# Kernel tuning notes

Measured on AMD Instinct MI355X. Metric: run time of the kernel, lower is better.

## Reference

```python
import jax, jax.numpy as jnp
import numpy as np

B, CI, CO, H, W, K = 8, 256, 256, 64, 64, 3


def _conv(x, w, b, stride, pad):
    y = jax.lax.conv_general_dilated(x, w, (stride, stride), [(pad, pad), (pad, pad)],
                                     dimension_numbers=('NCHW', 'OIHW', 'NCHW'))
    return y + b[None, :, None, None]


def _bn(x, g, b, eps=1e-5):
    m = jnp.mean(x, axis=(0, 2, 3), keepdims=True)
    v = jnp.var(x, axis=(0, 2, 3), keepdims=True)
    return (x - m) * jax.lax.rsqrt(v + eps) * g[None, :, None, None] + b[None, :, None, None]


def _deform_conv(x, offset, mask, w, b, stride=1, pad=1, k=3):
    # Modulated deformable conv v2 (torchvision deform_conv2d semantics).
    Bn, C, Hh, Ww = x.shape
    Ho = (Hh + 2 * pad - k) // stride + 1
    Wo = (Ww + 2 * pad - k) // stride + 1
    kk = jnp.arange(k * k)
    ky = (kk // k).astype(x.dtype)
    kx = (kk % k).astype(x.dtype)
    base_y = (jnp.arange(Ho) * stride - pad).astype(x.dtype)
    base_x = (jnp.arange(Wo) * stride - pad).astype(x.dtype)
    off = offset.reshape(Bn, k * k, 2, Ho, Wo)  # pairs (dy, dx) per kernel tap
    py = base_y[None, None, :, None] + ky[None, :, None, None] + off[:, :, 0]  # [B,K2,Ho,Wo]
    px = base_x[None, None, None, :] + kx[None, :, None, None] + off[:, :, 1]

    def sample(xb, pyb, pxb):  # xb [C,H,W]; pyb/pxb [K2,Ho,Wo]
        y0 = jnp.floor(pyb)
        x0 = jnp.floor(pxb)
        ly = pyb - y0
        lx = pxb - x0
        y0i = y0.astype(jnp.int32)
        x0i = x0.astype(jnp.int32)
        out = jnp.zeros((C, k * k, Ho, Wo), xb.dtype)
        for dy, dx, wgt in ((0, 0, (1 - ly) * (1 - lx)), (0, 1, (1 - ly) * lx),
                            (1, 0, ly * (1 - lx)), (1, 1, ly * lx)):
            yi = y0i + dy
            xi = x0i + dx
            valid = ((yi >= 0) & (yi < Hh) & (xi >= 0) & (xi < Ww)).astype(xb.dtype)
            yc = jnp.clip(yi, 0, Hh - 1)
            xc = jnp.clip(xi, 0, Ww - 1)
            out = out + xb[:, yc, xc] * (wgt * valid)[None]  # zero padding outside
        return out  # [C,K2,Ho,Wo]

    sampled = jax.vmap(sample)(x, py, px)          # [B,C,K2,Ho,Wo]
    sampled = sampled * mask[:, None]              # modulator mask [B,K2,Ho,Wo]
    wk = w.reshape(w.shape[0], C, k * k)
    return jnp.einsum('bcphw,ocp->bohw', sampled, wk) + b[None, :, None, None]


def setup_inputs() -> dict:
    key = jax.random.key(0)
    ks = jax.random.split(key, 16)
    n = jax.random.normal
    return {
        'x': n(ks[0], (B, CI, H, W), jnp.float32),
        'residual': jnp.zeros((B, CI, H, W), jnp.float32),  # unused (overwritten in forward)
        'w1': n(ks[1], (CO, CI, K, K), jnp.float32) * 0.05,
        'b1': n(ks[2], (CO,), jnp.float32) * 0.01,
        'g1': jnp.ones((CO,), jnp.float32),
        'bt1': jnp.zeros((CO,), jnp.float32),
        'w_off': n(ks[3], (2 * K * K, CO, K, K), jnp.float32) * 0.01,
        'b_off': jnp.zeros((2 * K * K,), jnp.float32),
        'w_mod': n(ks[4], (K * K, CO, K, K), jnp.float32) * 0.01,
        'b_mod': jnp.zeros((K * K,), jnp.float32),
        'w_d': n(ks[5], (CO, CO, K, K), jnp.float32) * 0.05,
        'b_d': jnp.zeros((CO,), jnp.float32),
        'g2': jnp.ones((CO,), jnp.float32),
        'bt2': jnp.zeros((CO,), jnp.float32),
        'w_ds': n(ks[6], (CO, CI, 1, 1), jnp.float32) * 0.05,
        'b_ds': jnp.zeros((CO,), jnp.float32),
        'g3': jnp.ones((CO,), jnp.float32),
        'bt3': jnp.zeros((CO,), jnp.float32),
    }


def reference(x, residual, w1, b1, g1, bt1, w_off, b_off, w_mod, b_mod,
              w_d, b_d, g2, bt2, w_ds, b_ds, g3, bt3):
    # residual arg is overwritten by x in the original forward
    out = jax.nn.relu(_bn(_conv(x, w1, b1, 1, 1), g1, bt1))
    offset = _conv(out, w_off, b_off, 1, 1)
    mask = 2.0 * jax.nn.sigmoid(_conv(out, w_mod, b_mod, 1, 1))
    out = _bn(_deform_conv(out, offset, mask, w_d, b_d, 1, 1, K), g2, bt2)
    res = _bn(_conv(x, w_ds, b_ds, 1, 0), g3, bt3)
    return jax.nn.relu(out + res)
```

## Files before the change

### kernel.cpp

```cpp
#include <hip/hip_runtime.h>
#include <math.h>

typedef __attribute__((ext_vector_type(8))) __bf16 bf16x8;
typedef __attribute__((ext_vector_type(4))) float f32x4;

#define PLANE 4096
#define IMG   1048576

__device__ inline ushort f2bf(float f) {
  uint u = __float_as_uint(f);
  u = (u + 0x7fffu + ((u >> 16) & 1u)) >> 16;
  return (ushort)u;
}

union frag_cv { uint4 u; bf16x8 v; };

__global__ void k_prep(const float* __restrict__ w1, const float* __restrict__ wd,
                       const float* __restrict__ woff, const float* __restrict__ wmod,
                       const float* __restrict__ wds,
                       ushort* __restrict__ wb1, ushort* __restrict__ wbd,
                       ushort* __restrict__ wbom, ushort* __restrict__ wbds) {
  int stride = gridDim.x * blockDim.x;
  int t0 = blockIdx.x * blockDim.x + threadIdx.x;
  for (int s = t0; s < 9 * 8 * 256 * 32; s += stride) {
    int kk = s & 31, co = (s >> 5) & 255, cic = (s >> 13) & 7, p = s >> 16;
    int ci = cic * 32 + kk;
    wb1[s] = f2bf(w1[(co * 256 + ci) * 9 + p]);
    wbd[s] = f2bf(wd[(co * 256 + ci) * 9 + p]);
  }
  for (int s = t0; s < 9 * 8 * 32 * 32; s += stride) {
    int kk = s & 31, co = (s >> 5) & 31, cic = (s >> 10) & 7, p = s >> 13;
    int ci = cic * 32 + kk;
    float v = 0.f;
    if (co < 18) v = woff[(co * 256 + ci) * 9 + p];
    else if (co < 27) v = wmod[((co - 18) * 256 + ci) * 9 + p];
    wbom[s] = f2bf(v);
  }
  for (int s = t0; s < 8 * 256 * 32; s += stride) {
    int kk = s & 31, co = (s >> 5) & 255, cic = s >> 13;
    wbds[s] = f2bf(wds[co * 256 + cic * 32 + kk]);
  }
}

__global__ __launch_bounds__(256) void k_x2nhwc(const float* __restrict__ x,
                                                ushort* __restrict__ xn) {
  __shared__ __align__(16) float sT[64 * 68];
  const int h = blockIdx.x, b = blockIdx.y, t = threadIdx.x;
  for (int chunk = 0; chunk < 4; ++chunk) {
    const int c0 = chunk * 64;
    {
      int w4 = (t & 15) * 4, cl = t >> 4;
      #pragma unroll
      for (int i = 0; i < 4; ++i) {
        int c = cl * 4 + i;
        float4 v = *(const float4*)&x[((b * 256 + c0 + c) * 64 + h) * 64 + w4];
        *(float4*)&sT[c * 68 + w4] = v;
      }
    }
    __syncthreads();
    {
      int w = t & 63, cg = t >> 6;
      #pragma unroll
      for (int i = 0; i < 2; ++i) {
        int cg2 = cg * 2 + i;
        uint ou[4];
        #pragma unroll
        for (int k2 = 0; k2 < 4; ++k2) {
          float lo = sT[(cg2 * 8 + k2 * 2) * 68 + w];
          float hi = sT[(cg2 * 8 + k2 * 2 + 1) * 68 + w];
          ou[k2] = (uint)f2bf(lo) | ((uint)f2bf(hi) << 16);
        }
        *(uint4*)&xn[(((b * 64 + h) * 64 + w) * 256) + c0 + cg2 * 8] = *(uint4*)ou;
      }
    }
    __syncthreads();
  }
}

template<int NCO, int NTAP, int MODE>
__global__ __launch_bounds__(256) void k_conv(const ushort* __restrict__ an,
                                              const ushort* __restrict__ wB,
                                              const float* __restrict__ boff,
                                              const float* __restrict__ bmod,
                                              float* __restrict__ out) {
  __shared__ __align__(16) ushort sA[64 * 264];
  __shared__ __align__(16) ushort sB[NCO * 40];
  const int h = blockIdx.x, b = blockIdx.y, t = threadIdx.x;
  const int lane = t & 63, wv = t >> 6;
  constexpr int MF = (NCO == 256) ? 4 : 1;
  constexpr int NF = (NCO == 256) ? 4 : 2;
  const int co_w = (NCO == 256) ? wv * 64 : 0;
  const int m0 = (NCO == 256) ? 0 : wv;
  f32x4 acc[MF][NF];
  #pragma unroll
  for (int m = 0; m < MF; ++m)
    #pragma unroll
    for (int n = 0; n < NF; ++n) acc[m][n] = (f32x4){0.f, 0.f, 0.f, 0.f};

  const int spx = t & 63, seg = t >> 6;
  for (int p = 0; p < NTAP; ++p) {
    {
      int ky = (NTAP == 9) ? p / 3 : 1, kx = (NTAP == 9) ? p % 3 : 1;
      int y = h + ky - 1;
      int sx = spx + kx - 1;
      bool ok = ((unsigned)y < 64u) && ((unsigned)sx < 64u);
      const ushort* src = an + (((b * 64 + y) * 64 + sx) * 256) + seg * 64;
      uint4 z = {0u, 0u, 0u, 0u};
      #pragma unroll
      for (int j = 0; j < 8; ++j) {
        uint4 v = z;
        if (ok) v = *(const uint4*)(src + j * 8);
        *(uint4*)&sA[spx * 264 + seg * 64 + j * 8] = v;
      }
    }
    for (int cic = 0; cic < 8; ++cic) {
      if (t < NCO) {
        const ushort* srcB = wB + ((p * 8 + cic) * NCO + t) * 32;
        #pragma unroll
        for (int j = 0; j < 4; ++j)
          *(uint4*)&sB[t * 40 + j * 8] = *(const uint4*)(srcB + j * 8);
      }
      __syncthreads();
      const int krow = lane >> 4;
      bf16x8 af[MF], bfr[NF];
      #pragma unroll
      for (int m = 0; m < MF; ++m) {
        frag_cv cv;
        cv.u = *(const uint4*)&sA[((m0 + m) * 16 + (lane & 15)) * 264 + cic * 32 + krow * 8];
        af[m] = cv.v;
      }
      #pragma unroll
      for (int n = 0; n < NF; ++n) {
        frag_cv cv;
        cv.u = *(const uint4*)&sB[(co_w + n * 16 + (lane & 15)) * 40 + krow * 8];
        bfr[n] = cv.v;
      }
      #pragma unroll
      for (int m = 0; m < MF; ++m)
        #pragma unroll
        for (int n = 0; n < NF; ++n)
          acc[m][n] = __builtin_amdgcn_mfma_f32_16x16x32_bf16(af[m], bfr[n], acc[m][n], 0, 0, 0);
      __syncthreads();
    }
  }
  const int row0 = (b * 64 + h) * 64;
  if (MODE == 0) {
    #pragma unroll
    for (int m = 0; m < MF; ++m) {
      int pxo = (m0 + m) * 16 + (lane >> 4) * 4;
      #pragma unroll
      for (int n = 0; n < NF; ++n) {
        int co = co_w + n * 16 + (lane & 15);
        #pragma unroll
        for (int r = 0; r < 4; ++r)
          out[(row0 + pxo + r) * 256 + co] = acc[m][n][r];
      }
    }
  } else {
    int pxo = m0 * 16 + (lane >> 4) * 4;
    #pragma unroll
    for (int n = 0; n < NF; ++n) {
      int co = n * 16 + (lane & 15);
      #pragma unroll
      for (int r = 0; r < 4; ++r) {
        float v = acc[0][n][r];
        float o;
        if (co < 18) o = v + boff[co];
        else if (co < 27) { float mm = v + bmod[co - 18]; o = 2.f / (1.f + __expf(-mm)); }
        else o = 0.f;
        out[(row0 + pxo + r) * 32 + co] = o;
      }
    }
  }
}

__global__ __launch_bounds__(256) void k_deform(const ushort* __restrict__ an,
                                                const float* __restrict__ om,
                                                const ushort* __restrict__ wB,
                                                float* __restrict__ out) {
  __shared__ __align__(16) ushort sA[64 * 264];
  __shared__ __align__(16) ushort sB[256 * 40];
  __shared__ __align__(16) float4 sW4[9 * 64];
  __shared__ uchar2 sYX[9 * 64];
  const int h = blockIdx.x, b = blockIdx.y, t = threadIdx.x;
  const int lane = t & 63, wv = t >> 6;
  for (int s = t; s < 576; s += 256) {
    int px = s & 63, p = s >> 6;
    int row = (b * 64 + h) * 64 + px;
    float dy = om[row * 32 + 2 * p];
    float dx = om[row * 32 + 2 * p + 1];
    float mk = om[row * 32 + 18 + p];
    float py = (float)(h + p / 3 - 1) + dy;
    float pxx = (float)(px + p % 3 - 1) + dx;
    float fy = floorf(py), fx = floorf(pxx);
    float ly = py - fy, lx = pxx - fx;
    int y0 = (int)fy, x0 = (int)fx;
    bool vy0 = ((unsigned)y0 < 64u), vy1 = ((unsigned)(y0 + 1) < 64u);
    bool vx0 = ((unsigned)x0 < 64u), vx1 = ((unsigned)(x0 + 1) < 64u);
    float4 wvv;
    wvv.x = (1.f - ly) * (1.f - lx) * mk * ((vy0 && vx0) ? 1.f : 0.f);
    wvv.y = (1.f - ly) * lx * mk * ((vy0 && vx1) ? 1.f : 0.f);
    wvv.z = ly * (1.f - lx) * mk * ((vy1 && vx0) ? 1.f : 0.f);
    wvv.w = ly * lx * mk * ((vy1 && vx1) ? 1.f : 0.f);
    sW4[p * 64 + px] = wvv;
    int yc = min(max(y0, -4), 250), xc = min(max(x0, -4), 250);
    sYX[p * 64 + px] = make_uchar2((unsigned char)(yc + 4), (unsigned char)(xc + 4));
  }
  __syncthreads();
  f32x4 acc[4][4];
  #pragma unroll
  for (int m = 0; m < 4; ++m)
    #pragma unroll
    for (int n = 0; n < 4; ++n) acc[m][n] = (f32x4){0.f, 0.f, 0.f, 0.f};

  const int spx = t & 63, seg = t >> 6;
  const ushort* base = an + (b * PLANE) * 256;
  for (int p = 0; p < 9; ++p) {
    {
      float4 wvv = sW4[p * 64 + spx];
      uchar2 yx = sYX[p * 64 + spx];
      int y0 = (int)yx.x - 4, x0 = (int)yx.y - 4;
      int y0c = min(max(y0, 0), 63), y1c = min(max(y0 + 1, 0), 63);
      int x0c = min(max(x0, 0), 63), x1c = min(max(x0 + 1, 0), 63);
      const ushort* r00 = base + (y0c * 64 + x0c) * 256 + seg * 64;
      const ushort* r01 = base + (y0c * 64 + x1c) * 256 + seg * 64;
      const ushort* r10 = base + (y1c * 64 + x0c) * 256 + seg * 64;
      const ushort* r11 = base + (y1c * 64 + x1c) * 256 + seg * 64;
      #pragma unroll
      for (int j = 0; j < 8; ++j) {
        uint4 c00 = *(const uint4*)(r00 + j * 8);
        uint4 c01 = *(const uint4*)(r01 + j * 8);
        uint4 c10 = *(const uint4*)(r10 + j * 8);
        uint4 c11 = *(const uint4*)(r11 + j * 8);
        uint ou[4];
        #pragma unroll
        for (int q = 0; q < 4; ++q) {
          uint a0 = ((const uint*)&c00)[q], a1 = ((const uint*)&c01)[q];
          uint a2 = ((const uint*)&c10)[q], a3 = ((const uint*)&c11)[q];
          float lo = wvv.x * __uint_as_float(a0 << 16) + wvv.y * __uint_as_float(a1 << 16)
                   + wvv.z * __uint_as_float(a2 << 16) + wvv.w * __uint_as_float(a3 << 16);
          float hi = wvv.x * __uint_as_float(a0 & 0xffff0000u) + wvv.y * __uint_as_float(a1 & 0xffff0000u)
                   + wvv.z * __uint_as_float(a2 & 0xffff0000u) + wvv.w * __uint_as_float(a3 & 0xffff0000u);
          ou[q] = (uint)f2bf(lo) | ((uint)f2bf(hi) << 16);
        }
        *(uint4*)&sA[spx * 264 + seg * 64 + j * 8] = *(uint4*)ou;
      }
    }
    for (int cic = 0; cic < 8; ++cic) {
      {
        const ushort* srcB = wB + ((p * 8 + cic) * 256 + t) * 32;
        #pragma unroll
        for (int j = 0; j < 4; ++j)
          *(uint4*)&sB[t * 40 + j * 8] = *(const uint4*)(srcB + j * 8);
      }
      __syncthreads();
      const int krow = lane >> 4;
      bf16x8 af[4], bfr[4];
      #pragma unroll
      for (int m = 0; m < 4; ++m) {
        frag_cv cv;
        cv.u = *(const uint4*)&sA[(m * 16 + (lane & 15)) * 264 + cic * 32 + krow * 8];
        af[m] = cv.v;
      }
      #pragma unroll
      for (int n = 0; n < 4; ++n) {
        frag_cv cv;
        cv.u = *(const uint4*)&sB[(wv * 64 + n * 16 + (lane & 15)) * 40 + krow * 8];
        bfr[n] = cv.v;
      }
      #pragma unroll
      for (int m = 0; m < 4; ++m)
        #pragma unroll
        for (int n = 0; n < 4; ++n)
          acc[m][n] = __builtin_amdgcn_mfma_f32_16x16x32_bf16(af[m], bfr[n], acc[m][n], 0, 0, 0);
      __syncthreads();
    }
  }
  const int row0 = (b * 64 + h) * 64;
  #pragma unroll
  for (int m = 0; m < 4; ++m) {
    int pxo = m * 16 + (lane >> 4) * 4;
    #pragma unroll
    for (int n = 0; n < 4; ++n) {
      int co = wv * 64 + n * 16 + (lane & 15);
      #pragma unroll
      for (int r = 0; r < 4; ++r)
        out[(row0 + pxo + r) * 256 + co] = acc[m][n][r];
    }
  }
}

__global__ __launch_bounds__(256) void k_statA(const float* __restrict__ t, float* __restrict__ part) {
  const int c = threadIdx.x;
  const int base = blockIdx.x * 128;
  float s1 = 0.f, s2 = 0.f;
  for (int r = 0; r < 128; ++r) {
    float v = t[(base + r) * 256 + c];
    s1 += v; s2 += v * v;
  }
  part[blockIdx.x * 512 + c] = s1;
  part[blockIdx.x * 512 + 256 + c] = s2;
}
__global__ void k_statB(const float* __restrict__ part, const float* __restrict__ g,
                        const float* __restrict__ bt, float* __restrict__ scale,
                        float* __restrict__ shift) {
  const int c = threadIdx.x;
  float s1 = 0.f, s2 = 0.f;
  for (int r = 0; r < 256; ++r) { s1 += part[r * 512 + c]; s2 += part[r * 512 + 256 + c]; }
  const float inv = 1.f / 32768.f;
  float m = s1 * inv;
  float var = s2 * inv - m * m;
  float a = g[c] * rsqrtf(var + 1e-5f);
  scale[c] = a;
  shift[c] = bt[c] - m * a;
}

__global__ void k_bnrelu(const float* __restrict__ t, const float* __restrict__ scale,
                         const float* __restrict__ shift, ushort* __restrict__ o) {
  int stride = gridDim.x * blockDim.x;
  for (int i = blockIdx.x * blockDim.x + threadIdx.x; i < 8388608 / 4; i += stride) {
    float4 v = ((const float4*)t)[i];
    int c0 = (i & 63) * 4;
    float4 s = *(const float4*)&scale[c0];
    float4 sh = *(const float4*)&shift[c0];
    float q0 = fmaxf(v.x * s.x + sh.x, 0.f);
    float q1 = fmaxf(v.y * s.y + sh.y, 0.f);
    float q2 = fmaxf(v.z * s.z + sh.z, 0.f);
    float q3 = fmaxf(v.w * s.w + sh.w, 0.f);
    uint lo = (uint)f2bf(q0) | ((uint)f2bf(q1) << 16);
    uint hi = (uint)f2bf(q2) | ((uint)f2bf(q3) << 16);
    ((uint2*)o)[i] = make_uint2(lo, hi);
  }
}

__global__ __launch_bounds__(256) void k_final(const float* __restrict__ t2, const float* __restrict__ res,
                                               const float* __restrict__ s2p, const float* __restrict__ sh2p,
                                               const float* __restrict__ s3p, const float* __restrict__ sh3p,
                                               float* __restrict__ o) {
  __shared__ __align__(16) float sT[64 * 68];
  const int h = blockIdx.x, b = blockIdx.y, t = threadIdx.x;
  const int row0 = (b * 64 + h) * 64;
  for (int chunk = 0; chunk < 4; ++chunk) {
    const int c0 = chunk * 64;
    {
      int px = t >> 2, s4 = t & 3;
      int rbase = (row0 + px) * 256 + c0 + s4 * 16;
      #pragma unroll
      for (int j = 0; j < 4; ++j) {
        int cl = s4 * 16 + j * 4;
        float4 a = *(const float4*)&t2[rbase + j * 4];
        float4 r = *(const float4*)&res[rbase + j * 4];
        float4 sa = *(const float4*)&s2p[c0 + cl];
        float4 sha = *(const float4*)&sh2p[c0 + cl];
        float4 sb = *(const float4*)&s3p[c0 + cl];
        float4 shb = *(const float4*)&sh3p[c0 + cl];
        sT[(cl + 0) * 68 + px] = fmaxf(a.x * sa.x + sha.x + r.x * sb.x + shb.x, 0.f);
        sT[(cl + 1) * 68 + px] = fmaxf(a.y * sa.y + sha.y + r.y * sb.y + shb.y, 0.f);
        sT[(cl + 2) * 68 + px] = fmaxf(a.z * sa.z + sha.z + r.z * sb.z + shb.z, 0.f);
        sT[(cl + 3) * 68 + px] = fmaxf(a.w * sa.w + sha.w + r.w * sb.w + shb.w, 0.f);
      }
    }
    __syncthreads();
    {
      int cl = t & 63, wseg = t >> 6;
      int obase = ((b * 256 + c0 + cl) * 64 + h) * 64 + wseg * 16;
      #pragma unroll
      for (int j = 0; j < 4; ++j) {
        float4 q;
        q.x = sT[cl * 68 + wseg * 16 + j * 4 + 0];
        q.y = sT[cl * 68 + wseg * 16 + j * 4 + 1];
        q.z = sT[cl * 68 + wseg * 16 + j * 4 + 2];
        q.w = sT[cl * 68 + wseg * 16 + j * 4 + 3];
        *(float4*)&o[obase + j * 4] = q;
      }
    }
    __syncthreads();
  }
}

extern "C" void kernel_launch(void* const* d_in, const int* in_sizes, int n_in,
                              void* d_out, int out_size, void* d_ws, size_t ws_size,
                              hipStream_t stream) {
  const float* x    = (const float*)d_in[0];
  const float* w1   = (const float*)d_in[2];
  const float* g1   = (const float*)d_in[4];
  const float* bt1  = (const float*)d_in[5];
  const float* woff = (const float*)d_in[6];
  const float* boff = (const float*)d_in[7];
  const float* wmod = (const float*)d_in[8];
  const float* bmod = (const float*)d_in[9];
  const float* wd   = (const float*)d_in[10];
  const float* g2   = (const float*)d_in[12];
  const float* bt2  = (const float*)d_in[13];
  const float* wds  = (const float*)d_in[14];
  const float* g3   = (const float*)d_in[16];
  const float* bt3  = (const float*)d_in[17];

  float* ws = (float*)d_ws;
  ushort* wb1  = (ushort*)ws;
  ushort* wbd  = (ushort*)(ws + 294912);
  ushort* wbom = (ushort*)(ws + 589824);
  ushort* wbds = (ushort*)(ws + 626688);
  float*  SC   = ws + 659456;
  float*  part = ws + 661504;
  ushort* xn   = (ushort*)(ws + 792576);
  ushort* out1 = (ushort*)(ws + 4986880);
  float*  t1   = ws + 9181184;
  float*  t2   = ws + 17569792;
  float*  om   = ws + 25958400;
  float*  res  = t1;

  dim3 ghb(64, 8);
  k_prep<<<512, 256, 0, stream>>>(w1, wd, woff, wmod, wds, wb1, wbd, wbom, wbds);
  k_x2nhwc<<<ghb, 256, 0, stream>>>(x, xn);
  k_conv<256, 9, 0><<<ghb, 256, 0, stream>>>(xn, wb1, nullptr, nullptr, t1);
  k_statA<<<256, 256, 0, stream>>>(t1, part);
  k_statB<<<1, 256, 0, stream>>>(part, g1, bt1, SC, SC + 256);
  k_bnrelu<<<2048, 256, 0, stream>>>(t1, SC, SC + 256, out1);
  k_conv<32, 9, 1><<<ghb, 256, 0, stream>>>(out1, wbom, boff, bmod, om);
  k_deform<<<ghb, 256, 0, stream>>>(out1, om, wbd, t2);
  k_statA<<<256, 256, 0, stream>>>(t2, part);
  k_statB<<<1, 256, 0, stream>>>(part, g2, bt2, SC + 512, SC + 768);
  k_conv<256, 1, 0><<<ghb, 256, 0, stream>>>(xn, wbds, nullptr, nullptr, res);
  k_statA<<<256, 256, 0, stream>>>(res, part);
  k_statB<<<1, 256, 0, stream>>>(part, g3, bt3, SC + 1024, SC + 1280);
  k_final<<<ghb, 256, 0, stream>>>(t2, res, SC + 512, SC + 768, SC + 1024, SC + 1280, (float*)d_out);
}
```

Before: 525.6 us.

## Fuse BN stats into conv epilogues, store bf16 intermediates, double-buffer weight tiles

The conv and deform kernels now compute per-block channel sums and sums of squares in their epilogues, which removes the separate k_statA passes. Intermediate activations (t1, t2, res) are stored as bf16 instead of fp32, halving their memory traffic. Weight tiles are double-buffered in shared memory with register prefetch, which cuts one barrier per K-step. The offset/mask conv now processes two rows per block. The risks are extra bf16 rounding of pre-BN values and higher shared memory and register use, which may lower occupancy.

```diff
diff --git a/kernel.cpp b/kernel.cpp
--- a/kernel.cpp
+++ b/kernel.cpp
@@ -77,98 +77,211 @@
   }
 }
 
-template<int NCO, int NTAP, int MODE>
-__global__ __launch_bounds__(256) void k_conv(const ushort* __restrict__ an,
-                                              const ushort* __restrict__ wB,
-                                              const float* __restrict__ boff,
-                                              const float* __restrict__ bmod,
-                                              float* __restrict__ out) {
+template<int NTAP>
+__global__ __launch_bounds__(256) void k_convbig(const ushort* __restrict__ an,
+                                                 const ushort* __restrict__ wB,
+                                                 ushort* __restrict__ ob,
+                                                 float* __restrict__ part) {
   __shared__ __align__(16) ushort sA[64 * 264];
-  __shared__ __align__(16) ushort sB[NCO * 40];
+  __shared__ __align__(16) ushort sB[2][256 * 40];
   const int h = blockIdx.x, b = blockIdx.y, t = threadIdx.x;
   const int lane = t & 63, wv = t >> 6;
-  constexpr int MF = (NCO == 256) ? 4 : 1;
-  constexpr int NF = (NCO == 256) ? 4 : 2;
-  const int co_w = (NCO == 256) ? wv * 64 : 0;
-  const int m0 = (NCO == 256) ? 0 : wv;
-  f32x4 acc[MF][NF];
-  #pragma unroll
-  for (int m = 0; m < MF; ++m)
-    #pragma unroll
-    for (int n = 0; n < NF; ++n) acc[m][n] = (f32x4){0.f, 0.f, 0.f, 0.f};
-
   const int spx = t & 63, seg = t >> 6;
+  f32x4 acc[4][4];
+  #pragma unroll
+  for (int m = 0; m < 4; ++m)
+    #pragma unroll
+    for (int n = 0; n < 4; ++n) acc[m][n] = (f32x4){0.f, 0.f, 0.f, 0.f};
+
+  uint4 aR[8], bR[4];
+  auto loadA = [&](int p) {
+    int ky = (NTAP == 9) ? p / 3 : 1, kx = (NTAP == 9) ? p % 3 : 1;
+    int y = h + ky - 1, sx = spx + kx - 1;
+    bool ok = ((unsigned)y < 64u) && ((unsigned)sx < 64u);
+    const ushort* src = an + (((b * 64 + y) * 64 + sx) * 256) + seg * 64;
+    #pragma unroll
+    for (int j = 0; j < 8; ++j) {
+      uint4 v = {0u, 0u, 0u, 0u};
+      if (ok) v = *(const uint4*)(src + j * 8);
+      aR[j] = v;
+    }
+  };
+  auto writeA = [&]() {
+    #pragma unroll
+    for (int j = 0; j < 8; ++j)
+      *(uint4*)&sA[spx * 264 + seg * 64 + j * 8] = aR[j];
+  };
+  auto loadB = [&](int s) {
+    const ushort* srcB = wB + (s * 256 + t) * 32;
+    #pragma unroll
+    for (int j = 0; j < 4; ++j) bR[j] = *(const uint4*)(srcB + j * 8);
+  };
+  auto writeB = [&](int buf) {
+    #pragma unroll
+    for (int j = 0; j < 4; ++j)
+      *(uint4*)&sB[buf][t * 40 + j * 8] = bR[j];
+  };
+
+  loadA(0); writeA();
+  loadB(0); writeB(0);
+  __syncthreads();
+  int buf = 0;
   for (int p = 0; p < NTAP; ++p) {
-    {
-      int ky = (NTAP == 9) ? p / 3 : 1, kx = (NTAP == 9) ? p % 3 : 1;
-      int y = h + ky - 1;
-      int sx = spx + kx - 1;
+    #pragma unroll
+    for (int cic = 0; cic < 8; ++cic) {
+      const int s = p * 8 + cic;
+      const bool last = (s == NTAP * 8 - 1);
+      const bool tapEnd = (cic == 7) && (p + 1 < NTAP);
+      if (!last) loadB(s + 1);
+      if (tapEnd) loadA(p + 1);
+      const int krow = lane >> 4;
+      bf16x8 af[4], bfr[4];
+      #pragma unroll
+      for (int m = 0; m < 4; ++m) {
+        frag_cv cv;
+        cv.u = *(const uint4*)&sA[(m * 16 + (lane & 15)) * 264 + cic * 32 + krow * 8];
+        af[m] = cv.v;
+      }
+      #pragma unroll
+      for (int n = 0; n < 4; ++n) {
+        frag_cv cv;
+        cv.u = *(const uint4*)&sB[buf][(wv * 64 + n * 16 + (lane & 15)) * 40 + krow * 8];
+        bfr[n] = cv.v;
+      }
+      #pragma unroll
+      for (int m = 0; m < 4; ++m)
+        #pragma unroll
+        for (int n = 0; n < 4; ++n)
+          acc[m][n] = __builtin_amdgcn_mfma_f32_16x16x32_bf16(af[m], bfr[n], acc[m][n], 0, 0, 0);
+      if (!last) writeB(buf ^ 1);
+      __syncthreads();
+      buf ^= 1;
+      if (tapEnd) { writeA(); __syncthreads(); }
+    }
+  }
+  const int row0 = (b * 64 + h) * 64;
+  #pragma unroll
+  for (int m = 0; m < 4; ++m) {
+    int pxo = m * 16 + (lane >> 4) * 4;
+    #pragma unroll
+    for (int n = 0; n < 4; ++n) {
+      int co = wv * 64 + n * 16 + (lane & 15);
+      #pragma unroll
+      for (int r = 0; r < 4; ++r)
+        ob[(row0 + pxo + r) * 256 + co] = f2bf(acc[m][n][r]);
+    }
+  }
+  const int blk = b * 64 + h;
+  #pragma unroll
+  for (int n = 0; n < 4; ++n) {
+    float s1 = 0.f, s2 = 0.f;
+    #pragma unroll
+    for (int m = 0; m < 4; ++m)
+      #pragma unroll
+      for (int r = 0; r < 4; ++r) {
+        float v = acc[m][n][r];
+        s1 += v; s2 += v * v;
+      }
+    s1 += __shfl_xor(s1, 16); s1 += __shfl_xor(s1, 32);
+    s2 += __shfl_xor(s2, 16); s2 += __shfl_xor(s2, 32);
+    if (lane < 16) {
+      int co = wv * 64 + n * 16 + lane;
+      part[blk * 512 + co] = s1;
+      part[blk * 512 + 256 + co] = s2;
+    }
+  }
+}
+
+__global__ __launch_bounds__(256) void k_convom(const ushort* __restrict__ an,
+                                                const ushort* __restrict__ wB,
+                                                const float* __restrict__ boff,
+                                                const float* __restrict__ bmod,
+                                                float* __restrict__ om) {
+  __shared__ __align__(16) ushort sA[128 * 264];
+  __shared__ __align__(16) ushort sB[2][32 * 40];
+  const int h0 = blockIdx.x * 2, b = blockIdx.y, t = threadIdx.x;
+  const int lane = t & 63, wv = t >> 6;
+  const int spx = t & 63, seg = t >> 6;
+  f32x4 acc[2][2];
+  #pragma unroll
+  for (int m = 0; m < 2; ++m)
+    #pragma unroll
+    for (int n = 0; n < 2; ++n) acc[m][n] = (f32x4){0.f, 0.f, 0.f, 0.f};
+
+  uint2 bR;
+  auto stageA = [&](int p) {
+    int ky = p / 3, kx = p % 3;
+    #pragma unroll
+    for (int rr = 0; rr < 2; ++rr) {
+      int y = h0 + rr + ky - 1, sx = spx + kx - 1;
       bool ok = ((unsigned)y < 64u) && ((unsigned)sx < 64u);
       const ushort* src = an + (((b * 64 + y) * 64 + sx) * 256) + seg * 64;
-      uint4 z = {0u, 0u, 0u, 0u};
       #pragma unroll
       for (int j = 0; j < 8; ++j) {
-        uint4 v = z;
+        uint4 v = {0u, 0u, 0u, 0u};
         if (ok) v = *(const uint4*)(src + j * 8);
-        *(uint4*)&sA[spx * 264 + seg * 64 + j * 8] = v;
-      }
-    }
+        *(uint4*)&sA[(rr * 64 + spx) * 264 + seg * 64 + j * 8] = v;
+      }
+    }
+  };
+  auto loadB = [&](int s) { bR = *(const uint2*)(wB + s * 1024 + t * 4); };
+  auto writeB = [&](int buf) {
+    int co = t >> 3, c4 = (t & 7) * 4;
+    *(uint2*)&sB[buf][co * 40 + c4] = bR;
+  };
+
+  stageA(0);
+  loadB(0); writeB(0);
+  __syncthreads();
+  int buf = 0;
+  for (int p = 0; p < 9; ++p) {
+    #pragma unroll
     for (int cic = 0; cic < 8; ++cic) {
-      if (t < NCO) {
-        const ushort* srcB = wB + ((p * 8 + cic) * NCO + t) * 32;
+      const int s = p * 8 + cic;
+      const bool last = (s == 71);
+      const bool tapEnd = (cic == 7) && (p < 8);
+      if (!last) loadB(s + 1);
+      const int krow = lane >> 4;
+      bf16x8 af[2], bfr[2];
+      #pragma unroll
+      for (int m = 0; m < 2; ++m) {
+        frag_cv cv;
+        cv.u = *(const uint4*)&sA[((wv * 2 + m) * 16 + (lane & 15)) * 264 + cic * 32 + krow * 8];
+        af[m] = cv.v;
+      }
+      #pragma unroll
+      for (int n = 0; n < 2; ++n) {
+        frag_cv cv;
+        cv.u = *(const uint4*)&sB[buf][(n * 16 + (lane & 15)) * 40 + krow * 8];
+        bfr[n] = cv.v;
+      }
+      #pragma unroll
+      for (int m = 0; m < 2; ++m)
         #pragma unroll
-        for (int j = 0; j < 4; ++j)
-          *(uint4*)&sB[t * 40 + j * 8] = *(const uint4*)(srcB + j * 8);
-      }
+        for (int n = 0; n < 2; ++n)
+          acc[m][n] = __builtin_amdgcn_mfma_f32_16x16x32_bf16(af[m], bfr[n], acc[m][n], 0, 0, 0);
+      if (!last) writeB(buf ^ 1);
       __syncthreads();
-      const int krow = lane >> 4;
-      bf16x8 af[MF], bfr[NF];
-      #pragma unroll
-      for (int m = 0; m < MF; ++m) {
-        frag_cv cv;
-        cv.u = *(const uint4*)&sA[((m0 + m) * 16 + (lane & 15)) * 264 + cic * 32 + krow * 8];
-        af[m] = cv.v;
-      }
-      #pragma unroll
-      for (int n = 0; n < NF; ++n) {
-        frag_cv cv;
-        cv.u = *(const uint4*)&sB[(co_w + n * 16 + (lane & 15)) * 40 + krow * 8];
-        bfr[n] = cv.v;
-      }
-      #pragma unroll
-      for (int m = 0; m < MF; ++m)
-        #pragma unroll
-        for (int n = 0; n < NF; ++n)
-          acc[m][n] = __builtin_amdgcn_mfma_f32_16x16x32_bf16(af[m], bfr[n], acc[m][n], 0, 0, 0);
-      __syncthreads();
-    }
-  }
-  const int row0 = (b * 64 + h) * 64;
-  if (MODE == 0) {
-    #pragma unroll
-    for (int m = 0; m < MF; ++m) {
-      int pxo = (m0 + m) * 16 + (lane >> 4) * 4;
-      #pragma unroll
-      for (int n = 0; n < NF; ++n) {
-        int co = co_w + n * 16 + (lane & 15);
-        #pragma unroll
-        for (int r = 0; r < 4; ++r)
-          out[(row0 + pxo + r) * 256 + co] = acc[m][n][r];
-      }
-    }
-  } else {
-    int pxo = m0 * 16 + (lane >> 4) * 4;
-    #pragma unroll
-    for (int n = 0; n < NF; ++n) {
+      buf ^= 1;
+      if (tapEnd) { stageA(p + 1); __syncthreads(); }
+    }
+  }
+  #pragma unroll
+  for (int m = 0; m < 2; ++m) {
+    int pxf = (wv * 2 + m) * 16 + (lane >> 4) * 4;
+    #pragma unroll
+    for (int n = 0; n < 2; ++n) {
       int co = n * 16 + (lane & 15);
       #pragma unroll
       for (int r = 0; r < 4; ++r) {
-        float v = acc[0][n][r];
+        float v = acc[m][n][r];
+        int px = pxf + r;
+        int row = (b * 64 + h0 + (px >> 6)) * 64 + (px & 63);
         float o;
         if (co < 18) o = v + boff[co];
         else if (co < 27) { float mm = v + bmod[co - 18]; o = 2.f / (1.f + __expf(-mm)); }
         else o = 0.f;
-        out[(row0 + pxo + r) * 32 + co] = o;
+        om[row * 32 + co] = o;
       }
     }
   }
@@ -177,83 +290,86 @@
 __global__ __launch_bounds__(256) void k_deform(const ushort* __restrict__ an,
                                                 const float* __restrict__ om,
                                                 const ushort* __restrict__ wB,
-                                                float* __restrict__ out) {
+                                                ushort* __restrict__ ob,
+                                                float* __restrict__ part) {
   __shared__ __align__(16) ushort sA[64 * 264];
-  __shared__ __align__(16) ushort sB[256 * 40];
-  __shared__ __align__(16) float4 sW4[9 * 64];
-  __shared__ uchar2 sYX[9 * 64];
+  __shared__ __align__(16) ushort sB[2][256 * 40];
   const int h = blockIdx.x, b = blockIdx.y, t = threadIdx.x;
   const int lane = t & 63, wv = t >> 6;
-  for (int s = t; s < 576; s += 256) {
-    int px = s & 63, p = s >> 6;
-    int row = (b * 64 + h) * 64 + px;
+  const int spx = t & 63, seg = t >> 6;
+  f32x4 acc[4][4];
+  #pragma unroll
+  for (int m = 0; m < 4; ++m)
+    #pragma unroll
+    for (int n = 0; n < 4; ++n) acc[m][n] = (f32x4){0.f, 0.f, 0.f, 0.f};
+
+  const ushort* base = an + (size_t)b * PLANE * 256;
+  const int row = (b * 64 + h) * 64 + spx;
+  uint4 bR[4];
+
+  auto gatherA = [&](int p) {
     float dy = om[row * 32 + 2 * p];
     float dx = om[row * 32 + 2 * p + 1];
     float mk = om[row * 32 + 18 + p];
     float py = (float)(h + p / 3 - 1) + dy;
-    float pxx = (float)(px + p % 3 - 1) + dx;
+    float pxx = (float)(spx + p % 3 - 1) + dx;
     float fy = floorf(py), fx = floorf(pxx);
     float ly = py - fy, lx = pxx - fx;
     int y0 = (int)fy, x0 = (int)fx;
     bool vy0 = ((unsigned)y0 < 64u), vy1 = ((unsigned)(y0 + 1) < 64u);
     bool vx0 = ((unsigned)x0 < 64u), vx1 = ((unsigned)(x0 + 1) < 64u);
-    float4 wvv;
-    wvv.x = (1.f - ly) * (1.f - lx) * mk * ((vy0 && vx0) ? 1.f : 0.f);
-    wvv.y = (1.f - ly) * lx * mk * ((vy0 && vx1) ? 1.f : 0.f);
-    wvv.z = ly * (1.f - lx) * mk * ((vy1 && vx0) ? 1.f : 0.f);
-    wvv.w = ly * lx * mk * ((vy1 && vx1) ? 1.f : 0.f);
-    sW4[p * 64 + px] = wvv;
-    int yc = min(max(y0, -4), 250), xc = min(max(x0, -4), 250);
-    sYX[p * 64 + px] = make_uchar2((unsigned char)(yc + 4), (unsigned char)(xc + 4));
-  }
+    float w00 = (1.f - ly) * (1.f - lx) * mk * ((vy0 && vx0) ? 1.f : 0.f);
+    float w01 = (1.f - ly) * lx * mk * ((vy0 && vx1) ? 1.f : 0.f);
+    float w10 = ly * (1.f - lx) * mk * ((vy1 && vx0) ? 1.f : 0.f);
+    float w11 = ly * lx * mk * ((vy1 && vx1) ? 1.f : 0.f);
+    int y0c = min(max(y0, 0), 63), y1c = min(max(y0 + 1, 0), 63);
+    int x0c = min(max(x0, 0), 63), x1c = min(max(x0 + 1, 0), 63);
+    const ushort* r00 = base + (y0c * 64 + x0c) * 256 + seg * 64;
+    const ushort* r01 = base + (y0c * 64 + x1c) * 256 + seg * 64;
+    const ushort* r10 = base + (y1c * 64 + x0c) * 256 + seg * 64;
+    const ushort* r11 = base + (y1c * 64 + x1c) * 256 + seg * 64;
+    #pragma unroll
+    for (int j = 0; j < 8; ++j) {
+      uint4 c00 = *(const uint4*)(r00 + j * 8);
+      uint4 c01 = *(const uint4*)(r01 + j * 8);
+      uint4 c10 = *(const uint4*)(r10 + j * 8);
+      uint4 c11 = *(const uint4*)(r11 + j * 8);
+      uint ou[4];
+      #pragma unroll
+      for (int q = 0; q < 4; ++q) {
+        uint a0 = ((const uint*)&c00)[q], a1 = ((const uint*)&c01)[q];
+        uint a2 = ((const uint*)&c10)[q], a3 = ((const uint*)&c11)[q];
+        float lo = w00 * __uint_as_float(a0 << 16) + w01 * __uint_as_float(a1 << 16)
+                 + w10 * __uint_as_float(a2 << 16) + w11 * __uint_as_float(a3 << 16);
+        float hi = w00 * __uint_as_float(a0 & 0xffff0000u) + w01 * __uint_as_float(a1 & 0xffff0000u)
+                 + w10 * __uint_as_float(a2 & 0xffff0000u) + w11 * __uint_as_float(a3 & 0xffff0000u);
+        ou[q] = (uint)f2bf(lo) | ((uint)f2bf(hi) << 16);
+      }
+      *(uint4*)&sA[spx * 264 + seg * 64 + j * 8] = *(uint4*)ou;
+    }
+  };
+  auto loadB = [&](int s) {
+    const ushort* srcB = wB + (s * 256 + t) * 32;
+    #pragma unroll
+    for (int j = 0; j < 4; ++j) bR[j] = *(const uint4*)(srcB + j * 8);
+  };
+  auto writeB = [&](int buf) {
+    #pragma unroll
+    for (int j = 0; j < 4; ++j)
+      *(uint4*)&sB[buf][t * 40 + j * 8] = bR[j];
+  };
+
+  gatherA(0);
+  loadB(0); writeB(0);
   __syncthreads();
-  f32x4 acc[4][4];
-  #pragma unroll
-  for (int m = 0; m < 4; ++m)
-    #pragma unroll
-    for (int n = 0; n < 4; ++n) acc[m][n] = (f32x4){0.f, 0.f, 0.f, 0.f};
-
-  const int spx = t & 63, seg = t >> 6;
-  const ushort* base = an + (b * PLANE) * 256;
+  int buf = 0;
   for (int p = 0; p < 9; ++p) {
-    {
-      float4 wvv = sW4[p * 64 + spx];
-      uchar2 yx = sYX[p * 64 + spx];
-      int y0 = (int)yx.x - 4, x0 = (int)yx.y - 4;
-      int y0c = min(max(y0, 0), 63), y1c = min(max(y0 + 1, 0), 63);
-      int x0c = min(max(x0, 0), 63), x1c = min(max(x0 + 1, 0), 63);
-      const ushort* r00 = base + (y0c * 64 + x0c) * 256 + seg * 64;
-      const ushort* r01 = base + (y0c * 64 + x1c) * 256 + seg * 64;
-      const ushort* r10 = base + (y1c * 64 + x0c) * 256 + seg * 64;
-      const ushort* r11 = base + (y1c * 64 + x1c) * 256 + seg * 64;
-      #pragma unroll
-      for (int j = 0; j < 8; ++j) {
-        uint4 c00 = *(const uint4*)(r00 + j * 8);
-        uint4 c01 = *(const uint4*)(r01 + j * 8);
-        uint4 c10 = *(const uint4*)(r10 + j * 8);
-        uint4 c11 = *(const uint4*)(r11 + j * 8);
-        uint ou[4];
-        #pragma unroll
-        for (int q = 0; q < 4; ++q) {
-          uint a0 = ((const uint*)&c00)[q], a1 = ((const uint*)&c01)[q];
-          uint a2 = ((const uint*)&c10)[q], a3 = ((const uint*)&c11)[q];
-          float lo = wvv.x * __uint_as_float(a0 << 16) + wvv.y * __uint_as_float(a1 << 16)
-                   + wvv.z * __uint_as_float(a2 << 16) + wvv.w * __uint_as_float(a3 << 16);
-          float hi = wvv.x * __uint_as_float(a0 & 0xffff0000u) + wvv.y * __uint_as_float(a1 & 0xffff0000u)
-                   + wvv.z * __uint_as_float(a2 & 0xffff0000u) + wvv.w * __uint_as_float(a3 & 0xffff0000u);
-          ou[q] = (uint)f2bf(lo) | ((uint)f2bf(hi) << 16);
-        }
-        *(uint4*)&sA[spx * 264 + seg * 64 + j * 8] = *(uint4*)ou;
-      }
-    }
+    #pragma unroll
     for (int cic = 0; cic < 8; ++cic) {
-      {
-        const ushort* srcB = wB + ((p * 8 + cic) * 256 + t) * 32;
-        #pragma unroll
-        for (int j = 0; j < 4; ++j)
-          *(uint4*)&sB[t * 40 + j * 8] = *(const uint4*)(srcB + j * 8);
-      }
-      __syncthreads();
+      const int s = p * 8 + cic;
+      const bool last = (s == 71);
+      const bool tapEnd = (cic == 7) && (p < 8);
+      if (!last) loadB(s + 1);
       const int krow = lane >> 4;
       bf16x8 af[4], bfr[4];
       #pragma unroll
@@ -265,7 +381,7 @@
       #pragma unroll
       for (int n = 0; n < 4; ++n) {
         frag_cv cv;
-        cv.u = *(const uint4*)&sB[(wv * 64 + n * 16 + (lane & 15)) * 40 + krow * 8];
+        cv.u = *(const uint4*)&sB[buf][(wv * 64 + n * 16 + (lane & 15)) * 40 + krow * 8];
         bfr[n] = cv.v;
       }
       #pragma unroll
@@ -273,7 +389,10 @@
         #pragma unroll
         for (int n = 0; n < 4; ++n)
           acc[m][n] = __builtin_amdgcn_mfma_f32_16x16x32_bf16(af[m], bfr[n], acc[m][n], 0, 0, 0);
+      if (!last) writeB(buf ^ 1);
       __syncthreads();
+      buf ^= 1;
+      if (tapEnd) { gatherA(p + 1); __syncthreads(); }
     }
   }
   const int row0 = (b * 64 + h) * 64;
@@ -285,28 +404,37 @@
       int co = wv * 64 + n * 16 + (lane & 15);
       #pragma unroll
       for (int r = 0; r < 4; ++r)
-        out[(row0 + pxo + r) * 256 + co] = acc[m][n][r];
-    }
-  }
-}
-
-__global__ __launch_bounds__(256) void k_statA(const float* __restrict__ t, float* __restrict__ part) {
-  const int c = threadIdx.x;
-  const int base = blockIdx.x * 128;
-  float s1 = 0.f, s2 = 0.f;
-  for (int r = 0; r < 128; ++r) {
-    float v = t[(base + r) * 256 + c];
-    s1 += v; s2 += v * v;
-  }
-  part[blockIdx.x * 512 + c] = s1;
-  part[blockIdx.x * 512 + 256 + c] = s2;
-}
+        ob[(row0 + pxo + r) * 256 + co] = f2bf(acc[m][n][r]);
+    }
+  }
+  const int blk = b * 64 + h;
+  #pragma unroll
+  for (int n = 0; n < 4; ++n) {
+    float s1 = 0.f, s2 = 0.f;
+    #pragma unroll
+    for (int m = 0; m < 4; ++m)
+      #pragma unroll
+      for (int r = 0; r < 4; ++r) {
+        float v = acc[m][n][r];
+        s1 += v; s2 += v * v;
+      }
+    s1 += __shfl_xor(s1, 16); s1 += __shfl_xor(s1, 32);
+    s2 += __shfl_xor(s2, 16); s2 += __shfl_xor(s2, 32);
+    if (lane < 16) {
+      int co = wv * 64 + n * 16 + lane;
+      part[blk * 512 + co] = s1;
+      part[blk * 512 + 256 + co] = s2;
+    }
+  }
+}
+
+template<int R>
 __global__ void k_statB(const float* __restrict__ part, const float* __restrict__ g,
                         const float* __restrict__ bt, float* __restrict__ scale,
                         float* __restrict__ shift) {
   const int c = threadIdx.x;
   float s1 = 0.f, s2 = 0.f;
-  for (int r = 0; r < 256; ++r) { s1 += part[r * 512 + c]; s2 += part[r * 512 + 256 + c]; }
+  for (int r = 0; r < R; ++r) { s1 += part[r * 512 + c]; s2 += part[r * 512 + 256 + c]; }
   const float inv = 1.f / 32768.f;
   float m = s1 * inv;
   float var = s2 * inv - m * m;
@@ -315,25 +443,34 @@
   shift[c] = bt[c] - m * a;
 }
 
-__global__ void k_bnrelu(const float* __restrict__ t, const float* __restrict__ scale,
+__global__ void k_bnrelu(const ushort* __restrict__ t, const float* __restrict__ scale,
                          const float* __restrict__ shift, ushort* __restrict__ o) {
   int stride = gridDim.x * blockDim.x;
-  for (int i = blockIdx.x * blockDim.x + threadIdx.x; i < 8388608 / 4; i += stride) {
-    float4 v = ((const float4*)t)[i];
-    int c0 = (i & 63) * 4;
-    float4 s = *(const float4*)&scale[c0];
-    float4 sh = *(const float4*)&shift[c0];
-    float q0 = fmaxf(v.x * s.x + sh.x, 0.f);
-    float q1 = fmaxf(v.y * s.y + sh.y, 0.f);
-    float q2 = fmaxf(v.z * s.z + sh.z, 0.f);
-    float q3 = fmaxf(v.w * s.w + sh.w, 0.f);
-    uint lo = (uint)f2bf(q0) | ((uint)f2bf(q1) << 16);
-    uint hi = (uint)f2bf(q2) | ((uint)f2bf(q3) << 16);
-    ((uint2*)o)[i] = make_uint2(lo, hi);
-  }
-}
-
-__global__ __launch_bounds__(256) void k_final(const float* __restrict__ t2, const float* __restrict__ res,
+  for (int i = blockIdx.x * blockDim.x + threadIdx.x; i < 8388608 / 8; i += stride) {
+    uint4 v = ((const uint4*)t)[i];
+    int c0 = (i & 31) * 8;
+    float4 sa = *(const float4*)&scale[c0];
+    float4 sb = *(const float4*)&scale[c0 + 4];
+    float4 ha = *(const float4*)&shift[c0];
+    float4 hb = *(const float4*)&shift[c0 + 4];
+    float e0 = __uint_as_float(v.x << 16), e1 = __uint_as_float(v.x & 0xffff0000u);
+    float e2 = __uint_as_float(v.y << 16), e3 = __uint_as_float(v.y & 0xffff0000u);
+    float e4 = __uint_as_float(v.z << 16), e5 = __uint_as_float(v.z & 0xffff0000u);
+    float e6 = __uint_as_float(v.w << 16), e7 = __uint_as_float(v.w & 0xffff0000u);
+    float q0 = fmaxf(e0 * sa.x + ha.x, 0.f), q1 = fmaxf(e1 * sa.y + ha.y, 0.f);
+    float q2 = fmaxf(e2 * sa.z + ha.z, 0.f), q3 = fmaxf(e3 * sa.w + ha.w, 0.f);
+    float q4 = fmaxf(e4 * sb.x + hb.x, 0.f), q5 = fmaxf(e5 * sb.y + hb.y, 0.f);
+    float q6 = fmaxf(e6 * sb.z + hb.z, 0.f), q7 = fmaxf(e7 * sb.w + hb.w, 0.f);
+    uint4 ou;
+    ou.x = (uint)f2bf(q0) | ((uint)f2bf(q1) << 16);
+    ou.y = (uint)f2bf(q2) | ((uint)f2bf(q3) << 16);
+    ou.z = (uint)f2bf(q4) | ((uint)f2bf(q5) << 16);
+    ou.w = (uint)f2bf(q6) | ((uint)f2bf(q7) << 16);
+    ((uint4*)o)[i] = ou;
+  }
+}
+
+__global__ __launch_bounds__(256) void k_final(const ushort* __restrict__ t2, const ushort* __restrict__ res,
                                                const float* __restrict__ s2p, const float* __restrict__ sh2p,
                                                const float* __restrict__ s3p, const float* __restrict__ sh3p,
                                                float* __restrict__ o) {
@@ -344,20 +481,35 @@
     const int c0 = chunk * 64;
     {
       int px = t >> 2, s4 = t & 3;
-      int rbase = (row0 + px) * 256 + c0 + s4 * 16;
-      #pragma unroll
-      for (int j = 0; j < 4; ++j) {
-        int cl = s4 * 16 + j * 4;
-        float4 a = *(const float4*)&t2[rbase + j * 4];
-        float4 r = *(const float4*)&res[rbase + j * 4];
-        float4 sa = *(const float4*)&s2p[c0 + cl];
-        float4 sha = *(const float4*)&sh2p[c0 + cl];
-        float4 sb = *(const float4*)&s3p[c0 + cl];
-        float4 shb = *(const float4*)&sh3p[c0 + cl];
-        sT[(cl + 0) * 68 + px] = fmaxf(a.x * sa.x + sha.x + r.x * sb.x + shb.x, 0.f);
-        sT[(cl + 1) * 68 + px] = fmaxf(a.y * sa.y + sha.y + r.y * sb.y + shb.y, 0.f);
-        sT[(cl + 2) * 68 + px] = fmaxf(a.z * sa.z + sha.z + r.z * sb.z + shb.z, 0.f);
-        sT[(cl + 3) * 68 + px] = fmaxf(a.w * sa.w + sha.w + r.w * sb.w + shb.w, 0.f);
+      int cl = s4 * 16;
+      int rbase = (row0 + px) * 256 + c0 + cl;
+      uint4 a0 = *(const uint4*)&t2[rbase];
+      uint4 a1 = *(const uint4*)&t2[rbase + 8];
+      uint4 r0 = *(const uint4*)&res[rbase];
+      uint4 r1 = *(const uint4*)&res[rbase + 8];
+      float sav[16], shv[16], sbv[16], hbv[16];
+      #pragma unroll
+      for (int k = 0; k < 4; ++k) {
+        float4 x1 = *(const float4*)&s2p[c0 + cl + k * 4];
+        float4 x2 = *(const float4*)&sh2p[c0 + cl + k * 4];
+        float4 x3 = *(const float4*)&s3p[c0 + cl + k * 4];
+        float4 x4 = *(const float4*)&sh3p[c0 + cl + k * 4];
+        sav[k*4]=x1.x; sav[k*4+1]=x1.y; sav[k*4+2]=x1.z; sav[k*4+3]=x1.w;
+        shv[k*4]=x2.x; shv[k*4+1]=x2.y; shv[k*4+2]=x2.z; shv[k*4+3]=x2.w;
+        sbv[k*4]=x3.x; sbv[k*4+1]=x3.y; sbv[k*4+2]=x3.z; sbv[k*4+3]=x3.w;
+        hbv[k*4]=x4.x; hbv[k*4+1]=x4.y; hbv[k*4+2]=x4.z; hbv[k*4+3]=x4.w;
+      }
+      const uint* au = (const uint*)&a0;
+      const uint* ru = (const uint*)&r0;
+      #pragma unroll
+      for (int q = 0; q < 8; ++q) {
+        uint ua = (q < 4) ? au[q] : ((const uint*)&a1)[q - 4];
+        uint ur = (q < 4) ? ru[q] : ((const uint*)&r1)[q - 4];
+        float ae = __uint_as_float(ua << 16), ao = __uint_as_float(ua & 0xffff0000u);
+        float re = __uint_as_float(ur << 16), ro = __uint_as_float(ur & 0xffff0000u);
+        int ce = 2 * q, codd = 2 * q + 1;
+        sT[(cl + ce) * 68 + px] = fmaxf(ae * sav[ce] + shv[ce] + re * sbv[ce] + hbv[ce], 0.f);
+        sT[(cl + codd) * 68 + px] = fmaxf(ao * sav[codd] + shv[codd] + ro * sbv[codd] + hbv[codd], 0.f);
       }
     }
     __syncthreads();
@@ -397,32 +549,31 @@
   const float* bt3  = (const float*)d_in[17];
 
   float* ws = (float*)d_ws;
-  ushort* wb1  = (ushort*)ws;
-  ushort* wbd  = (ushort*)(ws + 294912);
-  ushort* wbom = (ushort*)(ws + 589824);
-  ushort* wbds = (ushort*)(ws + 626688);
-  float*  SC   = ws + 659456;
-  float*  part = ws + 661504;
-  ushort* xn   = (ushort*)(ws + 792576);
-  ushort* out1 = (ushort*)(ws + 4986880);
-  float*  t1   = ws + 9181184;
-  float*  t2   = ws + 17569792;
-  float*  om   = ws + 25958400;
-  float*  res  = t1;
+  ushort* wb1   = (ushort*)ws;
+  ushort* wbd   = (ushort*)(ws + 294912);
+  ushort* wbom  = (ushort*)(ws + 589824);
+  ushort* wbds  = (ushort*)(ws + 626688);
+  float*  SC    = ws + 659456;
+  float*  part1 = ws + 661504;
+  float*  part2 = ws + 923648;
+  float*  part3 = ws + 1185792;
+  ushort* xn    = (ushort*)(ws + 1447936);
+  ushort* out1  = (ushort*)(ws + 5642240);
+  ushort* t1b   = (ushort*)(ws + 9836544);
+  ushort* t2b   = (ushort*)(ws + 14030848);
+  ushort* resb  = (ushort*)(ws + 18225152);
+  float*  om    = ws + 22419456;
 
   dim3 ghb(64, 8);
   k_prep<<<512, 256, 0, stream>>>(w1, wd, woff, wmod, wds, wb1, wbd, wbom, wbds);
   k_x2nhwc<<<ghb, 256, 0, stream>>>(x, xn);
-  k_conv<256, 9, 0><<<ghb, 256, 0, stream>>>(xn, wb1, nullptr, nullptr, t1);
-  k_statA<<<256, 256, 0, stream>>>(t1, part);
-  k_statB<<<1, 256, 0, stream>>>(part, g1, bt1, SC, SC + 256);
-  k_bnrelu<<<2048, 256, 0, stream>>>(t1, SC, SC + 256, out1);
-  k_conv<32, 9, 1><<<ghb, 256, 0, stream>>>(out1, wbom, boff, bmod, om);
-  k_deform<<<ghb, 256, 0, stream>>>(out1, om, wbd, t2);
-  k_statA<<<256, 256, 0, stream>>>(t2, part);
-  k_statB<<<1, 256, 0, stream>>>(part, g2, bt2, SC + 512, SC + 768);
-  k_conv<256, 1, 0><<<ghb, 256, 0, stream>>>(xn, wbds, nullptr, nullptr, res);
-  k_statA<<<256, 256, 0, stream>>>(res, part);
-  k_statB<<<1, 256, 0, stream>>>(part, g3, bt3, SC + 1024, SC + 1280);
-  k_final<<<ghb, 256, 0, stream>>>(t2, res, SC + 512, SC + 768, SC + 1024, SC + 1280, (float*)d_out);
-}
+  k_convbig<9><<<ghb, 256, 0, stream>>>(xn, wb1, t1b, part1);
+  k_statB<512><<<1, 256, 0, stream>>>(part1, g1, bt1, SC, SC + 256);
+  k_bnrelu<<<2048, 256, 0, stream>>>(t1b, SC, SC + 256, out1);
+  k_convom<<<dim3(32, 8), 256, 0, stream>>>(out1, wbom, boff, bmod, om);
+  k_deform<<<ghb, 256, 0, stream>>>(out1, om, wbd, t2b, part2);
+  k_statB<512><<<1, 256, 0, stream>>>(part2, g2, bt2, SC + 512, SC + 768);
+  k_convbig<1><<<ghb, 256, 0, stream>>>(xn, wbds, resb, part3);
+  k_statB<512><<<1, 256, 0, stream>>>(part3, g3, bt3, SC + 1024, SC + 1280);
+  k_final<<<ghb, 256, 0, stream>>>(t2b, resb, SC + 512, SC + 768, SC + 1024, SC + 1280, (float*)d_out);
+}
```

Measured after the change: 706.9 us. +34.5%, slower.
